# Optimization experiments

Hardware: AMD Instinct MI355X
Metric: run time of the kernel (lower is better)

The kernel has to match this reference:

```python
import jax, jax.numpy as jnp
import numpy as np

EPS = 1e-5
NH_MHA = 8
NH_GCN = 4


def _ln(x, w, b):
    m = x.mean(-1, keepdims=True)
    v = ((x - m) ** 2).mean(-1, keepdims=True)
    return (x - m) * jax.lax.rsqrt(v + EPS) * w + b


def _mha(t, in_w, in_b, out_w, out_b):
    # torch nn.MultiheadAttention (batch_first, eval mode -> no dropout)
    B, N, C = t.shape
    hd = C // NH_MHA
    qkv = t @ in_w.T + in_b
    q, k, v = jnp.split(qkv, 3, axis=-1)
    q = q.reshape(B, N, NH_MHA, hd)
    k = k.reshape(B, N, NH_MHA, hd)
    v = v.reshape(B, N, NH_MHA, hd)
    s = jnp.einsum('bihd,bjhd->bhij', q, k) * (1.0 / np.sqrt(hd))
    a = jax.nn.softmax(s, axis=-1)
    o = jnp.einsum('bhij,bjhd->bihd', a, v).reshape(B, N, C)
    return o @ out_w.T + out_b


def _gcn(x, v_w, v_b, e1_w, e1_b, eln_w, eln_b, e2_w, e2_b, o_w, o_b, n_w, n_b):
    # GraphConvolutionNetwork.forward (query/key branches are computed but
    # unused in the original -> omitted, identical math)
    B, N, C = x.shape
    hd = C // NH_GCN
    # edge MLP: split first linear so the [B,N,N,2C] concat is never built
    w1a, w1b = e1_w[:, :C], e1_w[:, C:]
    e = (x @ w1a.T)[:, :, None, :] + (x @ w1b.T)[:, None, :, :] + e1_b  # [B,N,N,C]
    e = jax.nn.gelu(_ln(e, eln_w, eln_b), approximate=False)
    ew = e @ e2_w.T + e2_b                 # [B,Ni,Nj,H]
    adj = jax.nn.softmax(ew, axis=2)       # softmax over Nj (== dim=-1 after permute in torch)
    v = (x @ v_w.T + v_b).reshape(B, N, NH_GCN, hd)
    out = jnp.einsum('bijh,bjhd->bihd', adj, v).reshape(B, N, C)
    out = out @ o_w.T + o_b
    return _ln(out + x, n_w, n_b)          # in_features == out_features -> residual


def reference(x, mha_in_w, mha_in_b, mha_out_w, mha_out_b,
              g0_v_w, g0_v_b, g0_e1_w, g0_e1_b, g0_eln_w, g0_eln_b, g0_e2_w, g0_e2_b, g0_o_w, g0_o_b, g0_n_w, g0_n_b,
              g1_v_w, g1_v_b, g1_e1_w, g1_e1_b, g1_eln_w, g1_eln_b, g1_e2_w, g1_e2_b, g1_o_w, g1_o_b, g1_n_w, g1_n_b,
              n1_w, n1_b, n2_w, n2_b,
              f1_w, f1_b, fln_w, fln_b, f2_w, f2_b):
    B, C, H, W = x.shape
    tokens = x.reshape(B, C, H * W).transpose(0, 2, 1)  # b c h w -> b (h w) c
    attn = _mha(tokens, mha_in_w, mha_in_b, mha_out_w, mha_out_b)
    attn = _ln(attn + tokens, n1_w, n1_b)
    g = _gcn(attn, g0_v_w, g0_v_b, g0_e1_w, g0_e1_b, g0_eln_w, g0_eln_b, g0_e2_w, g0_e2_b, g0_o_w, g0_o_b, g0_n_w, g0_n_b)
    g = _gcn(g, g1_v_w, g1_v_b, g1_e1_w, g1_e1_b, g1_eln_w, g1_eln_b, g1_e2_w, g1_e2_b, g1_o_w, g1_o_b, g1_n_w, g1_n_b)
    g = _ln(g, n2_w, n2_b)
    cat = jnp.concatenate([attn, g], axis=-1)           # [B,N,2C]
    f = cat @ f1_w.T + f1_b
    f = jax.nn.gelu(_ln(f, fln_w, fln_b), approximate=False)
    f = f @ f2_w.T + f2_b
    out = tokens + f
    return out.transpose(0, 2, 1).reshape(B, C, H, W)


def setup_inputs() -> dict:
    key = jax.random.key(0)
    ks = jax.random.split(key, 8)
    B, C, H, W = 2, 128, 24, 24
    f32 = jnp.float32

    def w(k, shape):
        return jax.random.normal(k, shape, f32) * 0.02

    d = {"x": jax.random.normal(ks[0], (B, C, H, W), f32)}
    d["mha_in_w"] = w(ks[1], (3 * C, C)); d["mha_in_b"] = jnp.zeros((3 * C,), f32)
    d["mha_out_w"] = w(ks[2], (C, C)); d["mha_out_b"] = jnp.zeros((C,), f32)
    for i in range(2):
        kk = jax.random.split(ks[3 + i], 4)
        p = f"g{i}_"
        d[p + "v_w"] = w(kk[0], (C, C)); d[p + "v_b"] = jnp.zeros((C,), f32)
        d[p + "e1_w"] = w(kk[1], (C, 2 * C)); d[p + "e1_b"] = jnp.zeros((C,), f32)
        d[p + "eln_w"] = jnp.ones((C,), f32); d[p + "eln_b"] = jnp.zeros((C,), f32)
        d[p + "e2_w"] = w(kk[2], (NH_GCN, C)); d[p + "e2_b"] = jnp.zeros((NH_GCN,), f32)
        d[p + "o_w"] = w(kk[3], (C, C)); d[p + "o_b"] = jnp.zeros((C,), f32)
        d[p + "n_w"] = jnp.ones((C,), f32); d[p + "n_b"] = jnp.zeros((C,), f32)
    d["n1_w"] = jnp.ones((C,), f32); d["n1_b"] = jnp.zeros((C,), f32)
    d["n2_w"] = jnp.ones((C,), f32); d["n2_b"] = jnp.zeros((C,), f32)
    d["f1_w"] = w(ks[5], (C, 2 * C)); d["f1_b"] = jnp.zeros((C,), f32)
    d["fln_w"] = jnp.ones((C,), f32); d["fln_b"] = jnp.zeros((C,), f32)
    d["f2_w"] = w(ks[6], (C, C)); d["f2_b"] = jnp.zeros((C,), f32)
    return d
```

## Files before the change

### kernel.cpp

```cpp
#include <hip/hip_runtime.h>
#include <hip/hip_fp16.h>
#include <math.h>

#define NN 576
#define EPSV 1e-5f
#define PSTR 592

typedef _Float16 h2v __attribute__((ext_vector_type(2)));
__device__ __forceinline__ float fdot2f(__half2 a, __half2 b, float c) {
    return __builtin_amdgcn_fdot2(__builtin_bit_cast(h2v, a),
                                  __builtin_bit_cast(h2v, b), c, false);
}
__device__ __forceinline__ __half2 h2minv(__half2 a, __half2 b) {
    return __builtin_bit_cast(__half2,
        __builtin_elementwise_min(__builtin_bit_cast(h2v, a), __builtin_bit_cast(h2v, b)));
}
__device__ __forceinline__ __half2 h2maxv(__half2 a, __half2 b) {
    return __builtin_bit_cast(__half2,
        __builtin_elementwise_max(__builtin_bit_cast(h2v, a), __builtin_bit_cast(h2v, b)));
}

__device__ __forceinline__ float gelu_exact(float x) {
    return 0.5f * x * (1.0f + erff(x * 0.70710678118654752f));
}

__global__ void k_setup(const float* __restrict__ x, float* __restrict__ tok,
                        const float* __restrict__ mha_in_w,
                        const float* __restrict__ e1w0, const float* __restrict__ vw0,
                        const float* __restrict__ e1w1, const float* __restrict__ vw1,
                        const float* __restrict__ lnw0, const float* __restrict__ lnb0,
                        const float* __restrict__ e2w0,
                        const float* __restrict__ lnw1, const float* __restrict__ lnb1,
                        const float* __restrict__ e2w1,
                        float* __restrict__ wTq, float* __restrict__ wT0,
                        float* __restrict__ wT1, __half* __restrict__ wh) {
    const int which = blockIdx.y;
    const int idx = blockIdx.x * 256 + threadIdx.x;
    if (which < 2) {
        if (idx < NN * 128) {
            int n = idx >> 7, c = idx & 127;
            tok[(size_t)which * NN * 128 + idx] = x[((size_t)which * 128 + c) * NN + n];
        }
        return;
    }
    if (which == 5) {
        if (idx < 1536) {
            int l = idx / 768, i2 = idx - l * 768;
            const float* lw = l ? lnw1 : lnw0;
            const float* lb = l ? lnb1 : lnb0;
            const float* e2 = l ? e2w1 : e2w0;
            float v;
            if (i2 < 128)      v = lw[i2];
            else if (i2 < 256) v = lb[i2 - 128];
            else               v = e2[i2 - 256];
            wh[idx] = __float2half(v);
        }
        return;
    }
    if (idx >= 49152) return;
    int k = idx / 384, o = idx - k * 384;
    if (which == 2) {
        wTq[idx] = mha_in_w[o * 128 + k];
    } else {
        const float* e1w = (which == 3) ? e1w0 : e1w1;
        const float* vw  = (which == 3) ? vw0  : vw1;
        float v;
        if (o < 128)      v = e1w[o * 256 + k];
        else if (o < 256) v = e1w[(o - 128) * 256 + 128 + k];
        else              v = vw[(o - 256) * 128 + k];
        ((which == 3) ? wT0 : wT1)[idx] = v;
    }
}

template<bool CENTER>
__global__ __launch_bounds__(384) void k_gemmT(
    const float* __restrict__ A, const float* __restrict__ wT,
    const float* __restrict__ b0, const float* __restrict__ b1, const float* __restrict__ b2,
    float* __restrict__ out)
{
    const int t = threadIdx.x;
    const int r0 = blockIdx.x * 4;
    __shared__ float a_s[4][132];
    if (t < 128) {
        float4 v = *(const float4*)(A + (size_t)(r0 + (t >> 5)) * 128 + (t & 31) * 4);
        *(float4*)&a_s[t >> 5][(t & 31) * 4] = v;
    }
    __syncthreads();
    float acc[4] = {0.f, 0.f, 0.f, 0.f};
    #pragma unroll 8
    for (int k = 0; k < 128; ++k) {
        float w = wT[(size_t)k * 384 + t];
        acc[0] += a_s[0][k] * w;
        acc[1] += a_s[1][k] * w;
        acc[2] += a_s[2][k] * w;
        acc[3] += a_s[3][k] * w;
    }
    const float* bp = (t < 128) ? b0 : ((t < 256) ? b1 : b2);
    float bv = bp ? bp[t & 127] : 0.f;
    #pragma unroll
    for (int r = 0; r < 4; ++r) acc[r] += bv;

    if (CENTER) {
        __shared__ float redc[6][4];
        const int wv = t >> 6, ln = t & 63;
        #pragma unroll
        for (int r = 0; r < 4; ++r) {
            float xr = acc[r];
            #pragma unroll
            for (int off = 32; off > 0; off >>= 1) xr += __shfl_xor(xr, off);
            if (ln == 0) redc[wv][r] = xr;
        }
        __syncthreads();
        if (t < 256) {
            const int ch = t >> 7;
            #pragma unroll
            for (int r = 0; r < 4; ++r) {
                float mean = (redc[2 * ch][r] + redc[2 * ch + 1][r]) * (1.0f / 128.0f);
                acc[r] -= mean;
            }
        }
    }
    if (t < 256) {
        #pragma unroll
        for (int r = 0; r < 4; ++r)
            ((__half*)(out + (size_t)(r0 + r) * 384))[t] = __float2half(acc[r]);
    } else {
        #pragma unroll
        for (int r = 0; r < 4; ++r)
            out[(size_t)(r0 + r) * 384 + t] = acc[r];
    }
}

__global__ __launch_bounds__(256) void k_score(
    const float* __restrict__ qkv, __half* __restrict__ sc)
{
    const int jt = blockIdx.x, it = blockIdx.y, b = blockIdx.z;
    const int i0 = it * 16, j0 = jt * 16;
    const int t = threadIdx.x;
    __shared__ __half q_s[16][136], k_s[16][136];
    for (int idx = t; idx < 512; idx += 256) {
        int tile = idx >> 8, r = (idx >> 4) & 15, cq = idx & 15;
        const __half* src = (const __half*)(qkv + (size_t)(b * NN + (tile ? j0 : i0) + r) * 384)
                            + (tile ? 128 : 0) + cq * 8;
        __half* dst = tile ? &k_s[r][cq * 8] : &q_s[r][cq * 8];
        *(uint4*)dst = *(const uint4*)src;
    }
    __syncthreads();
    const int ti = t >> 4, tj = t & 15;
    const uint4* qr = (const uint4*)q_s[ti];
    const uint4* kr = (const uint4*)k_s[tj];
    float acc[8] = {0.f,0.f,0.f,0.f,0.f,0.f,0.f,0.f};
    #pragma unroll
    for (int sstep = 0; sstep < 16; ++sstep) {
        uint4 q4 = qr[sstep], k4 = kr[sstep];
        const __half2* qh = (const __half2*)&q4;
        const __half2* kh = (const __half2*)&k4;
        #pragma unroll
        for (int p = 0; p < 4; ++p)
            acc[sstep >> 1] = fdot2f(qh[p], kh[p], acc[sstep >> 1]);
    }
    __half2 h[4];
    #pragma unroll
    for (int p = 0; p < 4; ++p)
        h[p] = __floats2half2_rn(acc[2 * p] * 0.25f, acc[2 * p + 1] * 0.25f);
    *(uint4*)(sc + ((size_t)(b * NN + i0 + ti) * NN + j0 + tj) * 8) = *(uint4*)h;
}

__global__ __launch_bounds__(256) void k_edge(
    const float* __restrict__ qkv, const __half* __restrict__ wh,
    const float* __restrict__ e2b, __half* __restrict__ ew)
{
    const int jt = blockIdx.x, it = blockIdx.y, b = blockIdx.z;
    const int i0 = it * 16, j0 = jt * 16;
    const int t = threadIdx.x;
    __shared__ __half ua_s[16][136], wb_s[16][136], wh_s[768];

    for (int idx = t; idx < 512; idx += 256) {
        int tile = idx >> 8, r = (idx >> 4) & 15, cq = idx & 15;
        const __half* src = (const __half*)(qkv + (size_t)(b * NN + (tile ? j0 : i0) + r) * 384)
                            + (tile ? 128 : 0) + cq * 8;
        __half* dst = tile ? &wb_s[r][cq * 8] : &ua_s[r][cq * 8];
        *(uint4*)dst = *(const uint4*)src;
    }
    if (t < 96) *(uint4*)&wh_s[t * 8] = *(const uint4*)&wh[t * 8];
    __syncthreads();

    const int ti = t >> 4, tj = t & 15;
    const uint4* uar = (const uint4*)ua_s[ti];
    const uint4* wbr = (const uint4*)wb_s[tj];

    float s2 = 0.f;
    #pragma unroll
    for (int sstep = 0; sstep < 16; ++sstep) {
        uint4 u4 = uar[sstep], w4 = wbr[sstep];
        const __half2* uh = (const __half2*)&u4;
        const __half2* whp = (const __half2*)&w4;
        #pragma unroll
        for (int p = 0; p < 4; ++p) {
            __half2 e = __hadd2(uh[p], whp[p]);
            s2 = fdot2f(e, e, s2);
        }
    }
    const float rstd = rsqrtf(s2 * (1.0f / 128.0f) + EPSV);
    const __half2 rh    = __float2half2_rn(rstd);
    const __half2 c851  = __float2half2_rn(0.851f);
    const __half2 smax  = __float2half2_rn(6.76f);
    const __half2 ca    = __float2half2_rn(0.983447f);
    const __half2 cb    = __float2half2_rn(-0.262113f);
    const __half2 cc    = __float2half2_rn(0.0474374f);
    const __half2 cd    = __float2half2_rn(-0.0032339f);
    const __half2 one2  = __float2half2_rn(1.0f);
    const __half2 none2 = __float2half2_rn(-1.0f);
    const __half2 hlf2  = __float2half2_rn(0.5f);

    float p0 = 0.f, p1 = 0.f, p2 = 0.f, p3 = 0.f;
    #pragma unroll 4
    for (int sstep = 0; sstep < 16; ++sstep) {
        uint4 u4 = uar[sstep], w4 = wbr[sstep];
        uint4 lw4 = *(const uint4*)&wh_s[sstep * 8];
        uint4 lb4 = *(const uint4*)&wh_s[128 + sstep * 8];
        uint4 q04 = *(const uint4*)&wh_s[256 + sstep * 8];
        uint4 q14 = *(const uint4*)&wh_s[384 + sstep * 8];
        uint4 q24 = *(const uint4*)&wh_s[512 + sstep * 8];
        uint4 q34 = *(const uint4*)&wh_s[640 + sstep * 8];
        const __half2* uh  = (const __half2*)&u4;
        const __half2* whp = (const __half2*)&w4;
        const __half2* lwh = (const __half2*)&lw4;
        const __half2* lbh = (const __half2*)&lb4;
        const __half2* q0h = (const __half2*)&q04;
        const __half2* q1h = (const __half2*)&q14;
        const __half2* q2h = (const __half2*)&q24;
        const __half2* q3h = (const __half2*)&q34;
        #pragma unroll
        for (int p = 0; p < 4; ++p) {
            __half2 e   = __hadd2(uh[p], whp[p]);
            __half2 t1  = __hmul2(e, lwh[p]);
            __half2 nrm = __hfma2(t1, rh, lbh[p]);
            __half2 u   = __hmul2(nrm, c851);
            __half2 s   = __hmul2(u, u);
            s  = h2minv(s, smax);
            __half2 f   = __hfma2(s, cd, cc);
            f  = __hfma2(f, s, cb);
            f  = __hfma2(f, s, ca);
            __half2 th  = __hmul2(u, f);
            th = h2minv(th, one2);
            th = h2maxv(th, none2);
            __half2 m   = __hfma2(th, hlf2, hlf2);
            __half2 g   = __hmul2(nrm, m);
            p0 = fdot2f(g, q0h[p], p0);
            p1 = fdot2f(g, q1h[p], p1);
            p2 = fdot2f(g, q2h[p], p2);
            p3 = fdot2f(g, q3h[p], p3);
        }
    }
    __half2 h01 = __floats2half2_rn(p0 + e2b[0], p1 + e2b[1]);
    __half2 h23 = __floats2half2_rn(p2 + e2b[2], p3 + e2b[3]);
    __half* dst = ew + ((size_t)(b * NN + i0 + ti) * NN + j0 + tj) * 4;
    *(__half2*)dst = h01;
    *(__half2*)(dst + 2) = h23;
}

template<int NH, bool FINAL>
__global__ __launch_bounds__(256) void k_agg(
    const float* __restrict__ resid, const float* __restrict__ vbuf,
    const __half* __restrict__ sc,
    const float* __restrict__ ow, const float* __restrict__ ob,
    const float* __restrict__ nw, const float* __restrict__ nb,
    float* __restrict__ outp,
    const float* __restrict__ tok, const float* __restrict__ attn,
    const float* __restrict__ n2w, const float* __restrict__ n2b,
    const float* __restrict__ f1w, const float* __restrict__ f1b,
    const float* __restrict__ flnw, const float* __restrict__ flnb,
    const float* __restrict__ f2w, const float* __restrict__ f2b,
    float* __restrict__ finout)
{
    constexpr int GL = 256 / NH;
    constexpr int NE = NN / GL;
    const int bi = blockIdx.x;
    const int b = bi / NN, i = bi - b * NN;
    const int t = threadIdx.x;

    __shared__ __half p_lds[NH * PSTR];
    __shared__ float st_i[NH];
    __shared__ float aggp[8][128];
    __shared__ float agg_s[128];
    __shared__ float op[2][128];
    __shared__ float red1[4], red2[4];
    __shared__ float cat_s[256], gl_s[128];
    __shared__ float red3[4], red4[4], red5[2], red6[2];

    const __half* srow = sc + (size_t)(b * NN + i) * NN * NH;

    {
        const int h = t / GL, jl = t % GL;
        float sv[NE];
        #pragma unroll
        for (int k = 0; k < NE; ++k)
            sv[k] = __half2float(srow[(size_t)(jl + k * GL) * NH + h]);
        float mx = -1e30f;
        #pragma unroll
        for (int k = 0; k < NE; ++k) mx = fmaxf(mx, sv[k]);
        #pragma unroll
        for (int off = GL / 2; off > 0; off >>= 1) mx = fmaxf(mx, __shfl_xor(mx, off));
        float sm = 0.f;
        #pragma unroll
        for (int k = 0; k < NE; ++k) {
            float e = __expf(sv[k] - mx);
            sm += e;
            p_lds[h * PSTR + jl + k * GL] = __float2half(e);
        }
        #pragma unroll
        for (int off = GL / 2; off > 0; off >>= 1) sm += __shfl_xor(sm, off);
        if (jl == 0) st_i[h] = 1.0f / sm;
    }
    __syncthreads();

    {
        const int c4 = (t & 31) * 4, jg = t >> 5;
        const int h2 = c4 >> ((NH == 8) ? 4 : 5);
        const float inv2 = st_i[h2];
        float4 acc = {0.f, 0.f, 0.f, 0.f};
        const float* vb = vbuf + 256 + c4;
        const __half* ph = p_lds + h2 * PSTR;
        #pragma unroll 4
        for (int j = jg; j < NN; j += 8) {
            float p = __half2float(ph[j]);
            const float4 v4 = *(const float4*)(vb + (size_t)(b * NN + j) * 384);
            acc.x += p * v4.x; acc.y += p * v4.y; acc.z += p * v4.z; acc.w += p * v4.w;
        }
        acc.x *= inv2; acc.y *= inv2; acc.z *= inv2; acc.w *= inv2;
        *(float4*)&aggp[jg][c4] = acc;
    }
    __syncthreads();
    if (t < 128) {
        float s = 0.f;
        #pragma unroll
        for (int gq = 0; gq < 8; ++gq) s += aggp[gq][t];
        agg_s[t] = s;
    }
    __syncthreads();

    {
        const int c = t & 127, half = t >> 7;
        float o = 0.f;
        const float4* wr = (const float4*)(ow + (size_t)c * 128 + half * 64);
        const float4* ar = (const float4*)(agg_s + half * 64);
        #pragma unroll
        for (int kq = 0; kq < 16; ++kq) {
            float4 w = wr[kq], a = ar[kq];
            o += w.x * a.x + w.y * a.y + w.z * a.z + w.w * a.w;
        }
        op[half][c] = o;
    }
    __syncthreads();
    const size_t row = (size_t)(b * NN + i) * 128;
    float val = 0.f;
    if (t < 128)
        val = op[0][t] + op[1][t] + ob[t] + resid[row + t];

    float s1 = val, s2 = val * val;
    #pragma unroll
    for (int off = 32; off > 0; off >>= 1) {
        s1 += __shfl_xor(s1, off);
        s2 += __shfl_xor(s2, off);
    }
    if ((t & 63) == 0) { red1[t >> 6] = s1; red2[t >> 6] = s2; }
    __syncthreads();
    float tot1 = red1[0] + red1[1] + red1[2] + red1[3];
    float tot2 = red2[0] + red2[1] + red2[2] + red2[3];
    float mean = tot1 * (1.0f / 128.0f);
    float var = tot2 * (1.0f / 128.0f) - mean * mean;
    float rstd = rsqrtf(var + EPSV);
    float gval = 0.f;
    if (t < 128) gval = (val - mean) * rstd * nw[t] + nb[t];

    if (!FINAL) {
        if (t < 128) outp[row + t] = gval;
        return;
    }

    {
        float a1 = gval, a2 = gval * gval;
        #pragma unroll
        for (int off = 32; off > 0; off >>= 1) { a1 += __shfl_xor(a1, off); a2 += __shfl_xor(a2, off); }
        if ((t & 63) == 0) { red3[t >> 6] = a1; red4[t >> 6] = a2; }
    }
    __syncthreads();
    {
        float m2 = (red3[0] + red3[1] + red3[2] + red3[3]) * (1.0f / 128.0f);
        float v2 = (red4[0] + red4[1] + red4[2] + red4[3]) * (1.0f / 128.0f) - m2 * m2;
        float r2 = rsqrtf(v2 + EPSV);
        if (t < 128) {
            cat_s[t] = attn[row + t];
            cat_s[128 + t] = (gval - m2) * r2 * n2w[t] + n2b[t];
        }
    }
    __syncthreads();
    {
        const int o = t & 127, half = t >> 7;
        float f = 0.f;
        const float4* wr = (const float4*)(f1w + (size_t)o * 256 + half * 128);
        const float4* cr = (const float4*)(cat_s + half * 128);
        #pragma unroll
        for (int kq = 0; kq < 32; ++kq) {
            float4 w = wr[kq], c = cr[kq];
            f += w.x * c.x + w.y * c.y + w.z * c.z + w.w * c.w;
        }
        op[half][o] = f;
    }
    __syncthreads();
    float fv = 0.f;
    if (t < 128) fv = op[0][t] + op[1][t] + f1b[t];
    {
        float a1 = fv, a2 = fv * fv;
        #pragma unroll
        for (int off = 32; off > 0; off >>= 1) { a1 += __shfl_xor(a1, off); a2 += __shfl_xor(a2, off); }
        if (t < 128 && (t & 63) == 0) { red5[t >> 6] = a1; red6[t >> 6] = a2; }
    }
    __syncthreads();
    {
        float m3 = (red5[0] + red5[1]) * (1.0f / 128.0f);
        float v3 = (red6[0] + red6[1]) * (1.0f / 128.0f) - m3 * m3;
        float r3 = rsqrtf(v3 + EPSV);
        if (t < 128) {
            float nrm = (fv - m3) * r3 * flnw[t] + flnb[t];
            gl_s[t] = gelu_exact(nrm);
        }
    }
    __syncthreads();
    {
        const int o = t & 127, half = t >> 7;
        float f = 0.f;
        const float4* wr = (const float4*)(f2w + (size_t)o * 128 + half * 64);
        const float4* gr = (const float4*)(gl_s + half * 64);
        #pragma unroll
        for (int kq = 0; kq < 16; ++kq) {
            float4 w = wr[kq], gg = gr[kq];
            f += w.x * gg.x + w.y * gg.y + w.z * gg.z + w.w * gg.w;
        }
        op[half][o] = f;
    }
    __syncthreads();
    if (t < 128)
        finout[((size_t)b * 128 + t) * NN + i] =
            tok[row + t] + op[0][t] + op[1][t] + f2b[t];
}

extern "C" void kernel_launch(void* const* d_in, const int* in_sizes, int n_in,
                              void* d_out, int out_size, void* d_ws, size_t ws_size,
                              hipStream_t stream) {
    const float* x         = (const float*)d_in[0];
    const float* mha_in_b  = (const float*)d_in[2];
    const float* mha_out_w = (const float*)d_in[3];
    const float* mha_out_b = (const float*)d_in[4];
    const float* gv_w[2]  = {(const float*)d_in[5],  (const float*)d_in[17]};
    const float* gv_b[2]  = {(const float*)d_in[6],  (const float*)d_in[18]};
    const float* ge1_w[2] = {(const float*)d_in[7],  (const float*)d_in[19]};
    const float* ge1_b[2] = {(const float*)d_in[8],  (const float*)d_in[20]};
    const float* geln_w[2]= {(const float*)d_in[9],  (const float*)d_in[21]};
    const float* geln_b[2]= {(const float*)d_in[10], (const float*)d_in[22]};
    const float* ge2_w[2] = {(const float*)d_in[11], (const float*)d_in[23]};
    const float* ge2_b[2] = {(const float*)d_in[12], (const float*)d_in[24]};
    const float* go_w[2]  = {(const float*)d_in[13], (const float*)d_in[25]};
    const float* go_b[2]  = {(const float*)d_in[14], (const float*)d_in[26]};
    const float* gn_w[2]  = {(const float*)d_in[15], (const float*)d_in[27]};
    const float* gn_b[2]  = {(const float*)d_in[16], (const float*)d_in[28]};
    const float* n1w = (const float*)d_in[29];
    const float* n1b = (const float*)d_in[30];
    const float* n2w = (const float*)d_in[31];
    const float* n2b = (const float*)d_in[32];
    const float* f1w = (const float*)d_in[33];
    const float* f1b = (const float*)d_in[34];
    const float* flnw = (const float*)d_in[35];
    const float* flnb = (const float*)d_in[36];
    const float* f2w = (const float*)d_in[37];
    const float* f2b = (const float*)d_in[38];

    float* ws     = (float*)d_ws;
    float* tokens = ws;
    float* attn   = tokens + 147456;
    float* g      = attn + 147456;
    float* qkv    = g + 147456;
    float* wTq    = qkv + 442368;
    float* wT0    = wTq + 49152;
    float* wT1    = wT0 + 49152;
    __half* wh    = (__half*)(wT1 + 49152);
    __half* sc    = wh + 2048;
    __half* ewh   = sc;

    k_setup<<<dim3(288, 6), 256, 0, stream>>>(x, tokens, (const float*)d_in[1],
        ge1_w[0], gv_w[0], ge1_w[1], gv_w[1],
        geln_w[0], geln_b[0], ge2_w[0],
        geln_w[1], geln_b[1], ge2_w[1],
        wTq, wT0, wT1, wh);

    k_gemmT<false><<<288, 384, 0, stream>>>(tokens, wTq,
        mha_in_b, mha_in_b + 128, mha_in_b + 256, qkv);
    k_score<<<dim3(36, 36, 2), 256, 0, stream>>>(qkv, sc);
    k_agg<8, false><<<1152, 256, 0, stream>>>(tokens, qkv, sc, mha_out_w, mha_out_b,
        n1w, n1b, attn,
        nullptr, nullptr, nullptr, nullptr, nullptr, nullptr, nullptr, nullptr,
        nullptr, nullptr, nullptr);

    for (int l = 0; l < 2; ++l) {
        const float* xin = (l == 0) ? attn : g;
        const float* wTl = (l == 0) ? wT0 : wT1;
        k_gemmT<true><<<288, 384, 0, stream>>>(xin, wTl,
            nullptr, ge1_b[l], gv_b[l], qkv);
        k_edge<<<dim3(36, 36, 2), 256, 0, stream>>>(qkv, wh + l * 768,
                                                    ge2_b[l], ewh);
        if (l == 0) {
            k_agg<4, false><<<1152, 256, 0, stream>>>(xin, qkv, ewh, go_w[l], go_b[l],
                gn_w[l], gn_b[l], g,
                nullptr, nullptr, nullptr, nullptr, nullptr, nullptr, nullptr, nullptr,
                nullptr, nullptr, nullptr);
        } else {
            k_agg<4, true><<<1152, 256, 0, stream>>>(xin, qkv, ewh, go_w[l], go_b[l],
                gn_w[l], gn_b[l], nullptr,
                tokens, attn, n2w, n2b, f1w, f1b, flnw, flnb, f2w, f2b,
                (float*)d_out);
        }
    }
}
```

Baseline: 215.6 us.

## Fuse next-layer projection GEMM into aggregation kernel and vectorize softmax loads

Each aggregation block computes the following GCN layer's e1/v projection from its freshly normalized row, so the two standalone projection GEMM launches are removed. The mean centering for the edge LayerNorm is folded into that fused step, and ping-pong qkv buffers keep reads and writes apart. The softmax now reads each row's head scores as one contiguous vector, with a block-wide reduction over a j-major LDS layout. In exchange each aggregation block does extra per-row GEMM work with poor weight reuse, and the first projection GEMM now uses 2 rows per block.

```diff
diff --git a/kernel.cpp b/kernel.cpp
--- a/kernel.cpp
+++ b/kernel.cpp
@@ -4,7 +4,6 @@
 
 #define NN 576
 #define EPSV 1e-5f
-#define PSTR 592
 
 typedef _Float16 h2v __attribute__((ext_vector_type(2)));
 __device__ __forceinline__ float fdot2f(__half2 a, __half2 b, float c) {
@@ -72,62 +71,35 @@
     }
 }
 
-template<bool CENTER>
 __global__ __launch_bounds__(384) void k_gemmT(
     const float* __restrict__ A, const float* __restrict__ wT,
     const float* __restrict__ b0, const float* __restrict__ b1, const float* __restrict__ b2,
     float* __restrict__ out)
 {
     const int t = threadIdx.x;
-    const int r0 = blockIdx.x * 4;
-    __shared__ float a_s[4][132];
-    if (t < 128) {
-        float4 v = *(const float4*)(A + (size_t)(r0 + (t >> 5)) * 128 + (t & 31) * 4);
-        *(float4*)&a_s[t >> 5][(t & 31) * 4] = v;
-    }
-    __syncthreads();
-    float acc[4] = {0.f, 0.f, 0.f, 0.f};
+    const int r0 = blockIdx.x * 2;
+    __shared__ float a_s[2][132];
+    if (t < 64) {
+        int r = t >> 5, cq = t & 31;
+        *(float4*)&a_s[r][cq * 4] = *(const float4*)(A + (size_t)(r0 + r) * 128 + cq * 4);
+    }
+    __syncthreads();
+    float acc0 = 0.f, acc1 = 0.f;
     #pragma unroll 8
     for (int k = 0; k < 128; ++k) {
         float w = wT[(size_t)k * 384 + t];
-        acc[0] += a_s[0][k] * w;
-        acc[1] += a_s[1][k] * w;
-        acc[2] += a_s[2][k] * w;
-        acc[3] += a_s[3][k] * w;
+        acc0 += a_s[0][k] * w;
+        acc1 += a_s[1][k] * w;
     }
     const float* bp = (t < 128) ? b0 : ((t < 256) ? b1 : b2);
     float bv = bp ? bp[t & 127] : 0.f;
-    #pragma unroll
-    for (int r = 0; r < 4; ++r) acc[r] += bv;
-
-    if (CENTER) {
-        __shared__ float redc[6][4];
-        const int wv = t >> 6, ln = t & 63;
-        #pragma unroll
-        for (int r = 0; r < 4; ++r) {
-            float xr = acc[r];
-            #pragma unroll
-            for (int off = 32; off > 0; off >>= 1) xr += __shfl_xor(xr, off);
-            if (ln == 0) redc[wv][r] = xr;
-        }
-        __syncthreads();
-        if (t < 256) {
-            const int ch = t >> 7;
-            #pragma unroll
-            for (int r = 0; r < 4; ++r) {
-                float mean = (redc[2 * ch][r] + redc[2 * ch + 1][r]) * (1.0f / 128.0f);
-                acc[r] -= mean;
-            }
-        }
-    }
+    acc0 += bv; acc1 += bv;
     if (t < 256) {
-        #pragma unroll
-        for (int r = 0; r < 4; ++r)
-            ((__half*)(out + (size_t)(r0 + r) * 384))[t] = __float2half(acc[r]);
+        ((__half*)(out + (size_t)(r0 + 0) * 384))[t] = __float2half(acc0);
+        ((__half*)(out + (size_t)(r0 + 1) * 384))[t] = __float2half(acc1);
     } else {
-        #pragma unroll
-        for (int r = 0; r < 4; ++r)
-            out[(size_t)(r0 + r) * 384 + t] = acc[r];
+        out[(size_t)(r0 + 0) * 384 + t] = acc0;
+        out[(size_t)(r0 + 1) * 384 + t] = acc1;
     }
 }
 
@@ -260,13 +232,15 @@
     *(__half2*)(dst + 2) = h23;
 }
 
-template<int NH, bool FINAL>
+template<int NH, bool PROJ, bool FINAL>
 __global__ __launch_bounds__(256) void k_agg(
     const float* __restrict__ resid, const float* __restrict__ vbuf,
     const __half* __restrict__ sc,
     const float* __restrict__ ow, const float* __restrict__ ob,
     const float* __restrict__ nw, const float* __restrict__ nb,
     float* __restrict__ outp,
+    const float* __restrict__ wTn, const float* __restrict__ e1bn,
+    const float* __restrict__ vbn, float* __restrict__ qkvout,
     const float* __restrict__ tok, const float* __restrict__ attn,
     const float* __restrict__ n2w, const float* __restrict__ n2b,
     const float* __restrict__ f1w, const float* __restrict__ f1b,
@@ -274,45 +248,92 @@
     const float* __restrict__ f2w, const float* __restrict__ f2b,
     float* __restrict__ finout)
 {
-    constexpr int GL = 256 / NH;
-    constexpr int NE = NN / GL;
     const int bi = blockIdx.x;
     const int b = bi / NN, i = bi - b * NN;
     const int t = threadIdx.x;
-
-    __shared__ __half p_lds[NH * PSTR];
+    const int wid = t >> 6, ln = t & 63;
+
+    __shared__ __half p_lds[NN * NH + 8];
     __shared__ float st_i[NH];
+    __shared__ float redm[4][NH], reds[4][NH];
     __shared__ float aggp[8][128];
     __shared__ float agg_s[128];
     __shared__ float op[2][128];
-    __shared__ float red1[4], red2[4];
+    __shared__ float red1[4], red2[4], redp[4];
     __shared__ float cat_s[256], gl_s[128];
-    __shared__ float red3[4], red4[4], red5[2], red6[2];
+    __shared__ float red5[2], red6[2];
 
     const __half* srow = sc + (size_t)(b * NN + i) * NN * NH;
 
-    {
-        const int h = t / GL, jl = t % GL;
-        float sv[NE];
-        #pragma unroll
-        for (int k = 0; k < NE; ++k)
-            sv[k] = __half2float(srow[(size_t)(jl + k * GL) * NH + h]);
-        float mx = -1e30f;
-        #pragma unroll
-        for (int k = 0; k < NE; ++k) mx = fmaxf(mx, sv[k]);
-        #pragma unroll
-        for (int off = GL / 2; off > 0; off >>= 1) mx = fmaxf(mx, __shfl_xor(mx, off));
-        float sm = 0.f;
-        #pragma unroll
-        for (int k = 0; k < NE; ++k) {
-            float e = __expf(sv[k] - mx);
-            sm += e;
-            p_lds[h * PSTR + jl + k * GL] = __float2half(e);
-        }
-        #pragma unroll
-        for (int off = GL / 2; off > 0; off >>= 1) sm += __shfl_xor(sm, off);
-        if (jl == 0) st_i[h] = 1.0f / sm;
-    }
+    float sv[3][NH];
+    #pragma unroll
+    for (int js = 0; js < 3; ++js) {
+        const int j = t + js * 256;
+        if (js == 2 && t >= 64) {
+            #pragma unroll
+            for (int h = 0; h < NH; ++h) sv[js][h] = -1e30f;
+        } else if (NH == 4) {
+            uint2 raw = *(const uint2*)(srow + (size_t)j * 4);
+            const __half2* hp = (const __half2*)&raw;
+            sv[js][0] = __low2float(hp[0]); sv[js][1] = __high2float(hp[0]);
+            sv[js][2] = __low2float(hp[1]); sv[js][3] = __high2float(hp[1]);
+        } else {
+            uint4 raw = *(const uint4*)(srow + (size_t)j * 8);
+            const __half2* hp = (const __half2*)&raw;
+            #pragma unroll
+            for (int p = 0; p < 4; ++p) {
+                sv[js][2 * p]     = __low2float(hp[p]);
+                sv[js][2 * p + 1] = __high2float(hp[p]);
+            }
+        }
+    }
+    #pragma unroll
+    for (int h = 0; h < NH; ++h) {
+        float m = fmaxf(fmaxf(sv[0][h], sv[1][h]), sv[2][h]);
+        #pragma unroll
+        for (int off = 32; off > 0; off >>= 1) m = fmaxf(m, __shfl_xor(m, off));
+        if (ln == 0) redm[wid][h] = m;
+    }
+    __syncthreads();
+    float mh[NH];
+    #pragma unroll
+    for (int h = 0; h < NH; ++h)
+        mh[h] = fmaxf(fmaxf(redm[0][h], redm[1][h]), fmaxf(redm[2][h], redm[3][h]));
+
+    float lsum[NH];
+    #pragma unroll
+    for (int h = 0; h < NH; ++h) lsum[h] = 0.f;
+    #pragma unroll
+    for (int js = 0; js < 3; ++js) {
+        const int j = t + js * 256;
+        if (js == 2 && t >= 64) continue;
+        float pv[NH];
+        #pragma unroll
+        for (int h = 0; h < NH; ++h) {
+            pv[h] = __expf(sv[js][h] - mh[h]);
+            lsum[h] += pv[h];
+        }
+        if (NH == 4) {
+            __half2 h01 = __floats2half2_rn(pv[0], pv[1]);
+            __half2 h23 = __floats2half2_rn(pv[2], pv[3]);
+            uint2 u; u.x = __builtin_bit_cast(unsigned, h01); u.y = __builtin_bit_cast(unsigned, h23);
+            *(uint2*)&p_lds[j * 4] = u;
+        } else {
+            __half2 hh[4];
+            #pragma unroll
+            for (int p = 0; p < 4; ++p) hh[p] = __floats2half2_rn(pv[2 * p], pv[2 * p + 1]);
+            *(uint4*)&p_lds[j * 8] = *(uint4*)hh;
+        }
+    }
+    #pragma unroll
+    for (int h = 0; h < NH; ++h) {
+        #pragma unroll
+        for (int off = 32; off > 0; off >>= 1) lsum[h] += __shfl_xor(lsum[h], off);
+        if (ln == 0) reds[wid][h] = lsum[h];
+    }
+    __syncthreads();
+    if (t < NH)
+        st_i[t] = 1.0f / (reds[0][t] + reds[1][t] + reds[2][t] + reds[3][t]);
     __syncthreads();
 
     {
@@ -321,10 +342,9 @@
         const float inv2 = st_i[h2];
         float4 acc = {0.f, 0.f, 0.f, 0.f};
         const float* vb = vbuf + 256 + c4;
-        const __half* ph = p_lds + h2 * PSTR;
         #pragma unroll 4
         for (int j = jg; j < NN; j += 8) {
-            float p = __half2float(ph[j]);
+            float p = __half2float(p_lds[j * NH + h2]);
             const float4 v4 = *(const float4*)(vb + (size_t)(b * NN + j) * 384);
             acc.x += p * v4.x; acc.y += p * v4.y; acc.z += p * v4.z; acc.w += p * v4.w;
         }
@@ -358,13 +378,13 @@
     if (t < 128)
         val = op[0][t] + op[1][t] + ob[t] + resid[row + t];
 
-    float s1 = val, s2 = val * val;
+    float s1 = val, s2r = val * val;
     #pragma unroll
     for (int off = 32; off > 0; off >>= 1) {
         s1 += __shfl_xor(s1, off);
-        s2 += __shfl_xor(s2, off);
-    }
-    if ((t & 63) == 0) { red1[t >> 6] = s1; red2[t >> 6] = s2; }
+        s2r += __shfl_xor(s2r, off);
+    }
+    if (ln == 0) { red1[wid] = s1; red2[wid] = s2r; }
     __syncthreads();
     float tot1 = red1[0] + red1[1] + red1[2] + red1[3];
     float tot2 = red2[0] + red2[1] + red2[2] + red2[3];
@@ -376,19 +396,44 @@
 
     if (!FINAL) {
         if (t < 128) outp[row + t] = gval;
+    }
+
+    if (PROJ) {
+        if (t < 128) agg_s[t] = gval;
+        __syncthreads();
+        float a0 = 0.f, a1 = 0.f;
+        const int o1 = 256 + (t & 127);
+        #pragma unroll 8
+        for (int k = 0; k < 128; ++k) {
+            float gk = agg_s[k];
+            a0 += gk * wTn[(size_t)k * 384 + t];
+            a1 += gk * wTn[(size_t)k * 384 + o1];
+        }
+        if (t >= 128) a0 += e1bn[t - 128];
+        float s = a0;
+        #pragma unroll
+        for (int off = 32; off > 0; off >>= 1) s += __shfl_xor(s, off);
+        if (ln == 0) redp[wid] = s;
+        __syncthreads();
+        float pmean = ((t < 128) ? (redp[0] + redp[1]) : (redp[2] + redp[3])) * (1.0f / 128.0f);
+        const size_t prow = (size_t)(b * NN + i) * 384;
+        ((__half*)(qkvout + prow))[t] = __float2half(a0 - pmean);
+        if (t < 128) qkvout[prow + 256 + t] = a1 + vbn[t];
         return;
     }
 
+    if (!FINAL) return;
+
     {
         float a1 = gval, a2 = gval * gval;
         #pragma unroll
         for (int off = 32; off > 0; off >>= 1) { a1 += __shfl_xor(a1, off); a2 += __shfl_xor(a2, off); }
-        if ((t & 63) == 0) { red3[t >> 6] = a1; red4[t >> 6] = a2; }
-    }
-    __syncthreads();
-    {
-        float m2 = (red3[0] + red3[1] + red3[2] + red3[3]) * (1.0f / 128.0f);
-        float v2 = (red4[0] + red4[1] + red4[2] + red4[3]) * (1.0f / 128.0f) - m2 * m2;
+        if (ln == 0) { redm[wid][0] = a1; reds[wid][0] = a2; }
+    }
+    __syncthreads();
+    {
+        float m2 = (redm[0][0] + redm[1][0] + redm[2][0] + redm[3][0]) * (1.0f / 128.0f);
+        float v2 = (reds[0][0] + reds[1][0] + reds[2][0] + reds[3][0]) * (1.0f / 128.0f) - m2 * m2;
         float r2 = rsqrtf(v2 + EPSV);
         if (t < 128) {
             cat_s[t] = attn[row + t];
@@ -415,7 +460,7 @@
         float a1 = fv, a2 = fv * fv;
         #pragma unroll
         for (int off = 32; off > 0; off >>= 1) { a1 += __shfl_xor(a1, off); a2 += __shfl_xor(a2, off); }
-        if (t < 128 && (t & 63) == 0) { red5[t >> 6] = a1; red6[t >> 6] = a2; }
+        if (t < 128 && ln == 0) { red5[wid] = a1; red6[wid] = a2; }
     }
     __syncthreads();
     {
@@ -480,8 +525,9 @@
     float* tokens = ws;
     float* attn   = tokens + 147456;
     float* g      = attn + 147456;
-    float* qkv    = g + 147456;
-    float* wTq    = qkv + 442368;
+    float* qkvA   = g + 147456;
+    float* qkvB   = qkvA + 442368;
+    float* wTq    = qkvB + 442368;
     float* wT0    = wTq + 49152;
     float* wT1    = wT0 + 49152;
     __half* wh    = (__half*)(wT1 + 49152);
@@ -494,31 +540,26 @@
         geln_w[1], geln_b[1], ge2_w[1],
         wTq, wT0, wT1, wh);
 
-    k_gemmT<false><<<288, 384, 0, stream>>>(tokens, wTq,
-        mha_in_b, mha_in_b + 128, mha_in_b + 256, qkv);
-    k_score<<<dim3(36, 36, 2), 256, 0, stream>>>(qkv, sc);
-    k_agg<8, false><<<1152, 256, 0, stream>>>(tokens, qkv, sc, mha_out_w, mha_out_b,
-        n1w, n1b, attn,
+    k_gemmT<<<576, 384, 0, stream>>>(tokens, wTq,
+        mha_in_b, mha_in_b + 128, mha_in_b + 256, qkvA);
+    k_score<<<dim3(36, 36, 2), 256, 0, stream>>>(qkvA, sc);
+    k_agg<8, true, false><<<1152, 256, 0, stream>>>(tokens, qkvA, sc,
+        mha_out_w, mha_out_b, n1w, n1b, attn,
+        wT0, ge1_b[0], gv_b[0], qkvB,
         nullptr, nullptr, nullptr, nullptr, nullptr, nullptr, nullptr, nullptr,
         nullptr, nullptr, nullptr);
 
-    for (int l = 0; l < 2; ++l) {
-        const float* xin = (l == 0) ? attn : g;
-        const float* wTl = (l == 0) ? wT0 : wT1;
-        k_gemmT<true><<<288, 384, 0, stream>>>(xin, wTl,
-            nullptr, ge1_b[l], gv_b[l], qkv);
-        k_edge<<<dim3(36, 36, 2), 256, 0, stream>>>(qkv, wh + l * 768,
-                                                    ge2_b[l], ewh);
-        if (l == 0) {
-            k_agg<4, false><<<1152, 256, 0, stream>>>(xin, qkv, ewh, go_w[l], go_b[l],
-                gn_w[l], gn_b[l], g,
-                nullptr, nullptr, nullptr, nullptr, nullptr, nullptr, nullptr, nullptr,
-                nullptr, nullptr, nullptr);
-        } else {
-            k_agg<4, true><<<1152, 256, 0, stream>>>(xin, qkv, ewh, go_w[l], go_b[l],
-                gn_w[l], gn_b[l], nullptr,
-                tokens, attn, n2w, n2b, f1w, f1b, flnw, flnb, f2w, f2b,
-                (float*)d_out);
-        }
-    }
-}
+    k_edge<<<dim3(36, 36, 2), 256, 0, stream>>>(qkvB, wh, ge2_b[0], ewh);
+    k_agg<4, true, false><<<1152, 256, 0, stream>>>(attn, qkvB, ewh,
+        go_w[0], go_b[0], gn_w[0], gn_b[0], g,
+        wT1, ge1_b[1], gv_b[1], qkvA,
+        nullptr, nullptr, nullptr, nullptr, nullptr, nullptr, nullptr, nullptr,
+        nullptr, nullptr, nullptr);
+
+    k_edge<<<dim3(36, 36, 2), 256, 0, stream>>>(qkvA, wh + 768, ge2_b[1], ewh);
+    k_agg<4, false, true><<<1152, 256, 0, stream>>>(g, qkvA, ewh,
+        go_w[1], go_b[1], gn_w[1], gn_b[1], nullptr,
+        nullptr, nullptr, nullptr, nullptr,
+        tokens, attn, n2w, n2b, f1w, f1b, flnw, flnb, f2w, f2b,
+        (float*)d_out);
+}
```

Measured after the change: 220.1 us. 1.02x slower.
